# Kernel tuning notes

Measured on AMD Instinct MI355X. Metric: run time of the kernel, lower is better.

Reference implementation:

```python
import jax, jax.numpy as jnp
import numpy as np

N = 8192
C_IN = 512
C_INTER = 128  # in_channels // unit_nums = 512 // 4


def setup_inputs() -> dict:
    key = jax.random.key(0)
    ks = jax.random.split(key, 6)
    x = jax.random.normal(ks[0], (N, C_IN), dtype=jnp.float32)
    # Linear weights init: normal(0, 0.01); biases zero. Stored as [in, out].
    Wg = 0.01 * jax.random.normal(ks[1], (C_IN, C_INTER), dtype=jnp.float32)
    Wt = 0.01 * jax.random.normal(ks[2], (C_IN, C_INTER), dtype=jnp.float32)
    Wp = 0.01 * jax.random.normal(ks[3], (C_IN, C_INTER), dtype=jnp.float32)
    bg = jnp.zeros((C_INTER,), dtype=jnp.float32)
    bt = jnp.zeros((C_INTER,), dtype=jnp.float32)
    bp = jnp.zeros((C_INTER,), dtype=jnp.float32)
    # 1x1 conv weight (1, 2*C_INTER, 1, 1) flattened: first half hits theta, second half phi
    wcat = 0.01 * jax.random.normal(ks[4], (2 * C_INTER,), dtype=jnp.float32)
    return {"x": x, "Wg": Wg, "bg": bg, "Wt": Wt, "bt": bt, "Wp": Wp, "bp": bp, "wcat": wcat}


def reference(x, Wg, bg, Wt, bt, Wp, bp, wcat):
    n = x.shape[0]
    g_x = x @ Wg + bg          # [N, C_inter]
    theta = x @ Wt + bt        # [N, C_inter]
    phi = x @ Wp + bp          # [N, C_inter]
    c = theta.shape[1]
    # 1x1 conv over cat([theta_i, phi_j]) == w1.theta_i + w2.phi_j (outer sum), then ReLU
    a = theta @ wcat[:c]       # [N]
    b = phi @ wcat[c:]         # [N]
    f = jax.nn.relu(a[:, None] + b[None, :])  # [N, N]
    z = (f / n) @ g_x          # [N, C_inter]
    return z
```

## Files before the change

### kernel.cpp

```cpp
#include <hip/hip_runtime.h>

#define C_IN   512
#define C_INT  128
#define NBUCK  8192
#define NSEG   256
#define BPS    (NBUCK / NSEG)

typedef short short8 __attribute__((ext_vector_type(8)));
typedef float floatx4 __attribute__((ext_vector_type(4)));


__device__ __forceinline__ int bucket_of(float v, float bmin, float inv_w) {
    float fk = (v - bmin) * inv_w;
    fk = fminf(fmaxf(fk, 0.f), (float)(NBUCK - 1));
    return (int)fk;
}

__device__ __forceinline__ short bf16rnd(float v) {
    unsigned u = __float_as_uint(v);
    return (short)((u + 0x7fffu + ((u >> 16) & 1u)) >> 16);
}


__global__ __launch_bounds__(256) void prep_kernel(
        const float* __restrict__ Wt, const float* __restrict__ Wp,
        const float* __restrict__ Wg, const float* __restrict__ wcat,
        const float* __restrict__ bt, const float* __restrict__ bp,
        float* __restrict__ ut, float* __restrict__ up, float* __restrict__ scal,
        unsigned short* __restrict__ WgT) {
    int t = threadIdx.x, bk = blockIdx.x;
    if (bk < 16) {
        const float* W  = (bk < 8) ? Wt : Wp;
        const float* wv = wcat + ((bk < 8) ? 0 : C_INT);
        float* dst      = (bk < 8) ? ut : up;
        int k = (bk & 7) * 64 + (t >> 2);
        int q = t & 3;
        const float4* row = (const float4*)(W + (size_t)k * C_INT);
        const float4* cv4 = (const float4*)wv;
        float s = 0.f;
        #pragma unroll
        for (int i = 0; i < 8; ++i) {
            float4 a = row[q * 8 + i];
            float4 c = cv4[q * 8 + i];
            s += a.x * c.x + a.y * c.y + a.z * c.z + a.w * c.w;
        }
        s += __shfl_xor(s, 1);
        s += __shfl_xor(s, 2);
        if (q == 0) dst[k] = s;
    } else if (bk == 16) {
        float s1p = (t < C_INT) ? bt[t] * wcat[t] : 0.f;
        float s2p = (t < C_INT) ? bp[t] * wcat[C_INT + t] : 0.f;
        for (int off = 32; off; off >>= 1) {
            s1p += __shfl_down(s1p, off);
            s2p += __shfl_down(s2p, off);
        }
        __shared__ float red[8];
        int w = t >> 6, lane = t & 63;
        if (lane == 0) { red[w] = s1p; red[4 + w] = s2p; }
        __syncthreads();
        if (t == 0) {
            scal[0] = red[0] + red[1] + red[2] + red[3];
            scal[1] = red[4] + red[5] + red[6] + red[7];
        }
    } else {
        __shared__ float tile[64][132];
        int kb = (bk - 17) * 64;
        #pragma unroll
        for (int it = 0; it < 8; ++it) {
            int idx = it * 256 + t;
            int r = idx >> 5, c4 = idx & 31;
            *(float4*)&tile[r][c4 * 4] =
                ((const float4*)(Wg + (size_t)(kb + r) * C_INT))[c4];
        }
        __syncthreads();
        int n = t & 127, kc = (t >> 7) * 32;
        unsigned pk[16];
        #pragma unroll
        for (int i = 0; i < 16; ++i) {
            unsigned lo = (unsigned short)bf16rnd(tile[kc + 2 * i][n]);
            unsigned hi = (unsigned short)bf16rnd(tile[kc + 2 * i + 1][n]);
            pk[i] = lo | (hi << 16);
        }
        uint4* dst = (uint4*)(WgT + (size_t)n * C_IN + kb + kc);
        #pragma unroll
        for (int i2 = 0; i2 < 4; ++i2) dst[i2] = *(uint4*)&pk[i2 * 4];
    }
}


#define RSTR 66

__global__ __launch_bounds__(256) void gemm_mfma(
        const float* __restrict__ x, const unsigned short* __restrict__ WgT,
        const float* __restrict__ bg,
        const float* __restrict__ ut, const float* __restrict__ up,
        const float* __restrict__ scal,
        _Float16* __restrict__ g, float* __restrict__ a, float* __restrict__ b) {
    __shared__ float red[3][20][RSTR];
    int tid = threadIdx.x;
    int lane = tid & 63, wv = tid >> 6;
    int bx = blockIdx.x;
    int i0 = (bx >> 1) * 16;
    int cg = bx & 1;
    int m = lane & 15, q = lane >> 4;
    floatx4 accg[4] = {};
    floatx4 accab = {};
    const float* xrow = x + (size_t)(i0 + m) * C_IN + q * 8;
    const float* absrc = (m == 0) ? ut : up;
    #pragma unroll
    for (int ks = 0; ks < 4; ++ks) {
        int k0 = (wv * 4 + ks) * 32;
        float4 f0 = *(const float4*)(xrow + k0);
        float4 f1 = *(const float4*)(xrow + k0 + 4);
        short8 af;
        af[0] = bf16rnd(f0.x); af[1] = bf16rnd(f0.y);
        af[2] = bf16rnd(f0.z); af[3] = bf16rnd(f0.w);
        af[4] = bf16rnd(f1.x); af[5] = bf16rnd(f1.y);
        af[6] = bf16rnd(f1.z); af[7] = bf16rnd(f1.w);
        if (cg == 0) {
            short8 abf = {};
            if (m < 2) {
                float4 u0 = *(const float4*)(absrc + k0 + q * 8);
                float4 u1 = *(const float4*)(absrc + k0 + q * 8 + 4);
                abf[0] = bf16rnd(u0.x); abf[1] = bf16rnd(u0.y);
                abf[2] = bf16rnd(u0.z); abf[3] = bf16rnd(u0.w);
                abf[4] = bf16rnd(u1.x); abf[5] = bf16rnd(u1.y);
                abf[6] = bf16rnd(u1.z); abf[7] = bf16rnd(u1.w);
            }
            accab = __builtin_amdgcn_mfma_f32_16x16x32_bf16(af, abf, accab, 0, 0, 0);
        }
        #pragma unroll
        for (int f = 0; f < 4; ++f) {
            short8 bfr = *(const short8*)(WgT + (size_t)(cg * 64 + f * 16 + m) * C_IN + k0 + q * 8);
            accg[f] = __builtin_amdgcn_mfma_f32_16x16x32_bf16(af, bfr, accg[f], 0, 0, 0);
        }
    }
    if (wv) {
        #pragma unroll
        for (int f = 0; f < 4; ++f)
            #pragma unroll
            for (int r = 0; r < 4; ++r)
                red[wv - 1][f * 4 + r][lane] = accg[f][r];
        #pragma unroll
        for (int r = 0; r < 4; ++r)
            red[wv - 1][16 + r][lane] = accab[r];
    }
    __syncthreads();
    if (wv == 0) {
        #pragma unroll
        for (int w = 0; w < 3; ++w) {
            #pragma unroll
            for (int f = 0; f < 4; ++f)
                #pragma unroll
                for (int r = 0; r < 4; ++r)
                    accg[f][r] += red[w][f * 4 + r][lane];
            #pragma unroll
            for (int r = 0; r < 4; ++r)
                accab[r] += red[w][16 + r][lane];
        }
        #pragma unroll
        for (int f = 0; f < 4; ++f) {
            int col = cg * 64 + f * 16 + m;
            float bgv = bg[col];
            #pragma unroll
            for (int r = 0; r < 4; ++r) {
                int row = i0 + q * 4 + r;
                g[(size_t)row * C_INT + col] = (_Float16)(accg[f][r] + bgv);
            }
        }
        if (cg == 0 && m < 2) {
            float off = m ? scal[1] : scal[0];
            float* dst = m ? b : a;
            #pragma unroll
            for (int r = 0; r < 4; ++r) dst[i0 + q * 4 + r] = accab[r] + off;
        }
    }
}


__global__ __launch_bounds__(1024) void postA_kernel(
        const _Float16* __restrict__ g, const float* __restrict__ b,
        float* __restrict__ scal,
        unsigned* __restrict__ offs_g, unsigned short* __restrict__ perm_g,
        float* __restrict__ bsort_g,
        float* __restrict__ seg1, float* __restrict__ seg2) {
    __shared__ unsigned oh[NBUCK / 2];
    __shared__ unsigned cur[NBUCK / 2];
    __shared__ unsigned short ls[8192];
    __shared__ unsigned wtu[16];
    __shared__ float smn[16], smx[16];
    __shared__ float part1[8][128], part2[8][128];
    int t = threadIdx.x, s = blockIdx.x;
    int lane = t & 63, wv = t >> 6;
    #pragma unroll
    for (int r = 0; r < 4; ++r) { oh[t + r * 1024] = 0u; cur[t + r * 1024] = 0u; }
    float bv[8];
    float mn = 1e30f, mx = -1e30f;
    #pragma unroll
    for (int r = 0; r < 8; ++r) {
        bv[r] = b[t + r * 1024];
        mn = fminf(mn, bv[r]); mx = fmaxf(mx, bv[r]);
    }
    for (int off = 32; off; off >>= 1) {
        mn = fminf(mn, __shfl_down(mn, off));
        mx = fmaxf(mx, __shfl_down(mx, off));
    }
    if (lane == 0) { smn[wv] = mn; smx[wv] = mx; }
    __syncthreads();
    if (t == 0) {
        float gmn = smn[0], gmx = smx[0];
        #pragma unroll
        for (int i = 1; i < 16; ++i) {
            gmn = fminf(gmn, smn[i]); gmx = fmaxf(gmx, smx[i]);
        }
        float range = gmx - gmn;
        float iw = (range > 1e-30f) ? (float)NBUCK / range : 0.f;
        smn[0] = gmn; smx[0] = iw;
        if (s == 0) { scal[4] = gmn; scal[5] = iw; }
    }
    __syncthreads();
    float bmin = smn[0], inv_w = smx[0];
    int kb[8];
    #pragma unroll
    for (int r = 0; r < 8; ++r) {
        kb[r] = bucket_of(bv[r], bmin, inv_w);
        atomicAdd(&oh[kb[r] >> 1], (kb[r] & 1) ? 0x10000u : 1u);
    }
    __syncthreads();
    unsigned h[8], p0 = 0;
    #pragma unroll
    for (int w = 0; w < 4; ++w) {
        unsigned word = oh[t * 4 + w];
        p0 += word & 0xffffu;  h[w * 2]     = p0;
        p0 += word >> 16;      h[w * 2 + 1] = p0;
    }
    unsigned v = p0;
    #pragma unroll
    for (int d = 1; d < 64; d <<= 1) {
        unsigned u = __shfl_up(v, d);
        if (lane >= d) v += u;
    }
    if (lane == 63) wtu[wv] = v;
    __syncthreads();
    if (t < 16) {
        unsigned w = wtu[t];
        #pragma unroll
        for (int d = 1; d < 16; d <<= 1) {
            unsigned u = __shfl_up(w, d);
            if (t >= d) w += u;
        }
        wtu[t] = w;
    }
    __syncthreads();
    unsigned base = (v - p0) + (wv ? wtu[wv - 1] : 0u);
    #pragma unroll
    for (int w = 0; w < 4; ++w) {
        unsigned lo = base + h[w * 2], hi = base + h[w * 2 + 1];
        oh[t * 4 + w] = lo | (hi << 16);
        if (s == 0) {
            offs_g[t * 8 + w * 2 + 1] = lo;
            offs_g[t * 8 + w * 2 + 2] = hi;
        }
    }
    if (s == 0 && t == 0) offs_g[0] = 0u;
    __syncthreads();
    #pragma unroll
    for (int r = 0; r < 8; ++r) {
        int j = t + r * 1024;
        int k = kb[r];
        unsigned st = 0u;
        if (k > 0) {
            unsigned word = oh[(k - 1) >> 1];
            st = ((k - 1) & 1) ? (word >> 16) : (word & 0xffffu);
        }
        unsigned old = atomicAdd(&cur[k >> 1], (k & 1) ? 0x10000u : 1u);
        unsigned pos = (k & 1) ? (old >> 16) : (old & 0xffffu);
        ls[st + pos] = (unsigned short)j;
    }
    __syncthreads();
    auto incl = [&](int kk) -> unsigned {
        unsigned word = oh[kk >> 1];
        return (kk & 1) ? (word >> 16) : (word & 0xffffu);
    };
    unsigned E0 = (s == 0) ? 0u : incl(s * BPS - 1);
    unsigned E1 = incl((s + 1) * BPS - 1);
    for (unsigned e = E0 + t; e < E1; e += 1024) {
        int j = ls[e];
        perm_g[e] = (unsigned short)j;
        bsort_g[e] = b[j];
    }
    int c = t & 127, p = t >> 7;
    float a1 = 0.f, a2 = 0.f;
    for (unsigned e = E0 + p; e < E1; e += 8) {
        int j = ls[e];
        float gv = (float)g[(size_t)j * C_INT + c];
        a1 += gv; a2 += b[j] * gv;
    }
    part1[p][c] = a1; part2[p][c] = a2;
    __syncthreads();
    if (p == 0) {
        float t1 = 0.f, t2 = 0.f;
        #pragma unroll
        for (int pp = 0; pp < 8; ++pp) { t1 += part1[pp][c]; t2 += part2[pp][c]; }
        seg1[s * C_INT + c] = t1;
        seg2[s * C_INT + c] = t2;
    }
}


__global__ __launch_bounds__(128) void postB_kernel(
        const _Float16* __restrict__ g, const unsigned* __restrict__ offs,
        const unsigned short* __restrict__ perm, const float* __restrict__ bsort,
        const float* __restrict__ seg1, const float* __restrict__ seg2,
        float* __restrict__ Pr1, float* __restrict__ Pr2) {
    __shared__ int pj[128];
    __shared__ float pb[128];
    int s = blockIdx.x, c = threadIdx.x;
    unsigned E0 = offs[s * BPS], E1 = offs[(s + 1) * BPS];
    float r1 = 0.f, r2 = 0.f;
    for (int s2 = s + 1; s2 < NSEG; ++s2) {
        r1 += seg1[s2 * C_INT + c];
        r2 += seg2[s2 * C_INT + c];
    }
    unsigned e = E1;
    while (e > E0) {
        unsigned cb = (e >= E0 + 128u) ? e - 128u : E0;
        unsigned cnt = e - cb;
        if ((unsigned)c < cnt) { pj[c] = perm[cb + c]; pb[c] = bsort[cb + c]; }
        __syncthreads();
        for (int r = (int)cnt - 1; r >= 0; --r) {
            float gv = (float)g[(size_t)pj[r] * C_INT + c];
            r1 += gv; r2 += pb[r] * gv;
            size_t idx = (size_t)(cb + r) * C_INT + c;
            Pr1[idx] = r1; Pr2[idx] = r2;
        }
        __syncthreads();
        e = cb;
    }
    if (s == 0) {
        Pr1[(size_t)8192 * C_INT + c] = 0.f;
        Pr2[(size_t)8192 * C_INT + c] = 0.f;
    }
}


__global__ __launch_bounds__(128) void out_kernel(
        const float* __restrict__ a, const float* __restrict__ scal,
        const _Float16* __restrict__ g,
        const unsigned* __restrict__ offs, const unsigned short* __restrict__ perm,
        const float* __restrict__ bsort,
        const float* __restrict__ Pr1, const float* __restrict__ Pr2,
        float* __restrict__ out, float inv_n) {
    __shared__ int pj[128];
    __shared__ float pb[128];
    int i = blockIdx.x, c = threadIdx.x;
    float ai = a[i], thr = -ai;
    float bmin = scal[4], inv_w = scal[5];
    int ki = bucket_of(thr, bmin, inv_w);
    unsigned e0 = offs[ki], e1 = offs[ki + 1];
    size_t base = (size_t)e1 * C_INT + c;
    float acc = ai * Pr1[base] + Pr2[base];
    for (unsigned be = e0; be < e1; be += 128) {
        unsigned cnt = min(128u, e1 - be);
        if ((unsigned)c < cnt) { pj[c] = perm[be + c]; pb[c] = bsort[be + c]; }
        __syncthreads();
        for (unsigned r = 0; r < cnt; ++r) {
            float bj = pb[r];
            if (bj > thr)
                acc += (ai + bj) * (float)g[(size_t)pj[r] * C_INT + c];
        }
        __syncthreads();
    }
    out[(size_t)i * C_INT + c] = acc * inv_n;
}


extern "C" void kernel_launch(void* const* d_in, const int* in_sizes, int n_in,
                              void* d_out, int out_size, void* d_ws, size_t ws_size,
                              hipStream_t stream) {
    const float* x    = (const float*)d_in[0];
    const float* Wg   = (const float*)d_in[1];
    const float* bg   = (const float*)d_in[2];
    const float* Wt   = (const float*)d_in[3];
    const float* bt   = (const float*)d_in[4];
    const float* Wp   = (const float*)d_in[5];
    const float* bp   = (const float*)d_in[6];
    const float* wcat = (const float*)d_in[7];
    float* out = (float*)d_out;
    int n = in_sizes[0] / C_IN;

    char* w = (char*)d_ws;
    size_t off = 0;
    auto alloc = [&](size_t bytes) -> void* {
        void* p = w + off;
        off += (bytes + 255) & ~(size_t)255;
        return p;
    };
    float*          ut    = (float*)alloc(C_IN * 4);
    float*          up    = (float*)alloc(C_IN * 4);
    float*          scal  = (float*)alloc(32);
    float*          a     = (float*)alloc((size_t)n * 4);
    float*          b     = (float*)alloc((size_t)n * 4);
    unsigned*       offs  = (unsigned*)alloc((size_t)(NBUCK + 1) * 4);
    unsigned short* perm  = (unsigned short*)alloc((size_t)n * 2);
    float*          bsort = (float*)alloc((size_t)n * 4);
    _Float16*       g     = (_Float16*)alloc((size_t)n * C_INT * 2);
    unsigned short* WgT   = (unsigned short*)alloc((size_t)C_INT * C_IN * 2);
    float*          seg1  = (float*)alloc((size_t)NSEG * C_INT * 4);
    float*          seg2  = (float*)alloc((size_t)NSEG * C_INT * 4);
    float*          Pr1   = (float*)alloc((size_t)(n + 1) * C_INT * 4);
    float*          Pr2   = (float*)alloc((size_t)(n + 1) * C_INT * 4);

    prep_kernel<<<25, 256, 0, stream>>>(Wt, Wp, Wg, wcat, bt, bp, ut, up, scal, WgT);
    gemm_mfma<<<n / 8, 256, 0, stream>>>(x, WgT, bg, ut, up, scal, g, a, b);
    postA_kernel<<<NSEG, 1024, 0, stream>>>(g, b, scal, offs, perm, bsort, seg1, seg2);
    postB_kernel<<<NSEG, 128, 0, stream>>>(g, offs, perm, bsort, seg1, seg2, Pr1, Pr2);
    out_kernel<<<n, 128, 0, stream>>>(a, scal, g, offs, perm, bsort, Pr1, Pr2,
                                      out, 1.0f / (float)n);
}
```

Before: 143.5 us.

## Fuse bucketing, suffix-prefix and output stages into one cooperative kernel

Merges postA, postB and out_kernel into a single cooperative kernel with 256 blocks of 1024 threads, separated by grid-wide syncs. This removes two kernel launches and the global round trip for scalars, and reuses the shared-memory sorted list. In the fused version the per-segment suffix scan runs on only 128 threads per block. The output stage now has 1024 threads handle 32 rows per block, down from 8192 blocks of 128 threads, which reduces parallelism and leaves the irregular bucket loops serialized per thread.

```diff
diff --git a/kernel.cpp b/kernel.cpp
--- a/kernel.cpp
+++ b/kernel.cpp
@@ -1,4 +1,7 @@
 #include <hip/hip_runtime.h>
+#include <hip/hip_cooperative_groups.h>
+
+namespace cg = cooperative_groups;
 
 #define C_IN   512
 #define C_INT  128
@@ -101,7 +104,7 @@
     int lane = tid & 63, wv = tid >> 6;
     int bx = blockIdx.x;
     int i0 = (bx >> 1) * 16;
-    int cg = bx & 1;
+    int cg0 = bx & 1;
     int m = lane & 15, q = lane >> 4;
     floatx4 accg[4] = {};
     floatx4 accab = {};
@@ -117,7 +120,7 @@
         af[2] = bf16rnd(f0.z); af[3] = bf16rnd(f0.w);
         af[4] = bf16rnd(f1.x); af[5] = bf16rnd(f1.y);
         af[6] = bf16rnd(f1.z); af[7] = bf16rnd(f1.w);
-        if (cg == 0) {
+        if (cg0 == 0) {
             short8 abf = {};
             if (m < 2) {
                 float4 u0 = *(const float4*)(absrc + k0 + q * 8);
@@ -131,7 +134,7 @@
         }
         #pragma unroll
         for (int f = 0; f < 4; ++f) {
-            short8 bfr = *(const short8*)(WgT + (size_t)(cg * 64 + f * 16 + m) * C_IN + k0 + q * 8);
+            short8 bfr = *(const short8*)(WgT + (size_t)(cg0 * 64 + f * 16 + m) * C_IN + k0 + q * 8);
             accg[f] = __builtin_amdgcn_mfma_f32_16x16x32_bf16(af, bfr, accg[f], 0, 0, 0);
         }
     }
@@ -160,7 +163,7 @@
         }
         #pragma unroll
         for (int f = 0; f < 4; ++f) {
-            int col = cg * 64 + f * 16 + m;
+            int col = cg0 * 64 + f * 16 + m;
             float bgv = bg[col];
             #pragma unroll
             for (int r = 0; r < 4; ++r) {
@@ -168,7 +171,7 @@
                 g[(size_t)row * C_INT + col] = (_Float16)(accg[f][r] + bgv);
             }
         }
-        if (cg == 0 && m < 2) {
+        if (cg0 == 0 && m < 2) {
             float off = m ? scal[1] : scal[0];
             float* dst = m ? b : a;
             #pragma unroll
@@ -178,12 +181,15 @@
 }
 
 
-__global__ __launch_bounds__(1024) void postA_kernel(
+__global__ __launch_bounds__(1024) void mega_kernel(
         const _Float16* __restrict__ g, const float* __restrict__ b,
-        float* __restrict__ scal,
+        const float* __restrict__ a,
         unsigned* __restrict__ offs_g, unsigned short* __restrict__ perm_g,
         float* __restrict__ bsort_g,
-        float* __restrict__ seg1, float* __restrict__ seg2) {
+        float* __restrict__ seg1, float* __restrict__ seg2,
+        float* __restrict__ Pr1, float* __restrict__ Pr2,
+        float* __restrict__ out, float inv_n) {
+    cg::grid_group grid = cg::this_grid();
     __shared__ unsigned oh[NBUCK / 2];
     __shared__ unsigned cur[NBUCK / 2];
     __shared__ unsigned short ls[8192];
@@ -192,6 +198,8 @@
     __shared__ float part1[8][128], part2[8][128];
     int t = threadIdx.x, s = blockIdx.x;
     int lane = t & 63, wv = t >> 6;
+    int c = t & 127, p = t >> 7;
+
     #pragma unroll
     for (int r = 0; r < 4; ++r) { oh[t + r * 1024] = 0u; cur[t + r * 1024] = 0u; }
     float bv[8];
@@ -216,7 +224,6 @@
         float range = gmx - gmn;
         float iw = (range > 1e-30f) ? (float)NBUCK / range : 0.f;
         smn[0] = gmn; smx[0] = iw;
-        if (s == 0) { scal[4] = gmn; scal[5] = iw; }
     }
     __syncthreads();
     float bmin = smn[0], inv_w = smx[0];
@@ -289,89 +296,69 @@
         perm_g[e] = (unsigned short)j;
         bsort_g[e] = b[j];
     }
-    int c = t & 127, p = t >> 7;
-    float a1 = 0.f, a2 = 0.f;
-    for (unsigned e = E0 + p; e < E1; e += 8) {
-        int j = ls[e];
-        float gv = (float)g[(size_t)j * C_INT + c];
-        a1 += gv; a2 += b[j] * gv;
-    }
-    part1[p][c] = a1; part2[p][c] = a2;
-    __syncthreads();
-    if (p == 0) {
-        float t1 = 0.f, t2 = 0.f;
-        #pragma unroll
-        for (int pp = 0; pp < 8; ++pp) { t1 += part1[pp][c]; t2 += part2[pp][c]; }
-        seg1[s * C_INT + c] = t1;
-        seg2[s * C_INT + c] = t2;
-    }
-}
-
-
-__global__ __launch_bounds__(128) void postB_kernel(
-        const _Float16* __restrict__ g, const unsigned* __restrict__ offs,
-        const unsigned short* __restrict__ perm, const float* __restrict__ bsort,
-        const float* __restrict__ seg1, const float* __restrict__ seg2,
-        float* __restrict__ Pr1, float* __restrict__ Pr2) {
-    __shared__ int pj[128];
-    __shared__ float pb[128];
-    int s = blockIdx.x, c = threadIdx.x;
-    unsigned E0 = offs[s * BPS], E1 = offs[(s + 1) * BPS];
-    float r1 = 0.f, r2 = 0.f;
-    for (int s2 = s + 1; s2 < NSEG; ++s2) {
-        r1 += seg1[s2 * C_INT + c];
-        r2 += seg2[s2 * C_INT + c];
-    }
-    unsigned e = E1;
-    while (e > E0) {
-        unsigned cb = (e >= E0 + 128u) ? e - 128u : E0;
-        unsigned cnt = e - cb;
-        if ((unsigned)c < cnt) { pj[c] = perm[cb + c]; pb[c] = bsort[cb + c]; }
+    {
+        float a1 = 0.f, a2 = 0.f;
+        for (unsigned e = E0 + p; e < E1; e += 8) {
+            int j = ls[e];
+            float gv = (float)g[(size_t)j * C_INT + c];
+            a1 += gv; a2 += b[j] * gv;
+        }
+        part1[p][c] = a1; part2[p][c] = a2;
         __syncthreads();
-        for (int r = (int)cnt - 1; r >= 0; --r) {
-            float gv = (float)g[(size_t)pj[r] * C_INT + c];
-            r1 += gv; r2 += pb[r] * gv;
-            size_t idx = (size_t)(cb + r) * C_INT + c;
-            Pr1[idx] = r1; Pr2[idx] = r2;
-        }
-        __syncthreads();
-        e = cb;
-    }
-    if (s == 0) {
-        Pr1[(size_t)8192 * C_INT + c] = 0.f;
-        Pr2[(size_t)8192 * C_INT + c] = 0.f;
-    }
-}
-
-
-__global__ __launch_bounds__(128) void out_kernel(
-        const float* __restrict__ a, const float* __restrict__ scal,
-        const _Float16* __restrict__ g,
-        const unsigned* __restrict__ offs, const unsigned short* __restrict__ perm,
-        const float* __restrict__ bsort,
-        const float* __restrict__ Pr1, const float* __restrict__ Pr2,
-        float* __restrict__ out, float inv_n) {
-    __shared__ int pj[128];
-    __shared__ float pb[128];
-    int i = blockIdx.x, c = threadIdx.x;
-    float ai = a[i], thr = -ai;
-    float bmin = scal[4], inv_w = scal[5];
-    int ki = bucket_of(thr, bmin, inv_w);
-    unsigned e0 = offs[ki], e1 = offs[ki + 1];
-    size_t base = (size_t)e1 * C_INT + c;
-    float acc = ai * Pr1[base] + Pr2[base];
-    for (unsigned be = e0; be < e1; be += 128) {
-        unsigned cnt = min(128u, e1 - be);
-        if ((unsigned)c < cnt) { pj[c] = perm[be + c]; pb[c] = bsort[be + c]; }
-        __syncthreads();
-        for (unsigned r = 0; r < cnt; ++r) {
-            float bj = pb[r];
-            if (bj > thr)
-                acc += (ai + bj) * (float)g[(size_t)pj[r] * C_INT + c];
-        }
-        __syncthreads();
-    }
-    out[(size_t)i * C_INT + c] = acc * inv_n;
+        if (p == 0) {
+            float t1 = 0.f, t2 = 0.f;
+            #pragma unroll
+            for (int pp = 0; pp < 8; ++pp) { t1 += part1[pp][c]; t2 += part2[pp][c]; }
+            seg1[s * C_INT + c] = t1;
+            seg2[s * C_INT + c] = t2;
+        }
+    }
+    grid.sync();
+
+    {
+        float r1 = 0.f, r2 = 0.f;
+        for (int s2 = s + 1 + p; s2 < NSEG; s2 += 8) {
+            r1 += seg1[s2 * C_INT + c];
+            r2 += seg2[s2 * C_INT + c];
+        }
+        part1[p][c] = r1; part2[p][c] = r2;
+    }
+    __syncthreads();
+    if (t < 128) {
+        float w1 = 0.f, w2 = 0.f;
+        #pragma unroll
+        for (int pp = 0; pp < 8; ++pp) { w1 += part1[pp][t]; w2 += part2[pp][t]; }
+        for (int e = (int)E1 - 1; e >= (int)E0; --e) {
+            int j = ls[e];
+            float gv = (float)g[(size_t)j * C_INT + t];
+            w1 += gv; w2 += b[j] * gv;
+            size_t idx = (size_t)e * C_INT + t;
+            Pr1[idx] = w1; Pr2[idx] = w2;
+        }
+        if (s == 0) {
+            Pr1[(size_t)8192 * C_INT + t] = 0.f;
+            Pr2[(size_t)8192 * C_INT + t] = 0.f;
+        }
+    }
+    grid.sync();
+
+    #pragma unroll
+    for (int batch = 0; batch < 4; ++batch) {
+        int i = s * 32 + batch * 8 + p;
+        float ai = a[i], thr = -ai;
+        int ki = bucket_of(thr, bmin, inv_w);
+        unsigned e0 = offs_g[ki], e1 = offs_g[ki + 1];
+        size_t pb = (size_t)e1 * C_INT + c;
+        float acc = ai * Pr1[pb] + Pr2[pb];
+        for (unsigned e = e0; e < e1; ++e) {
+            float bj = bsort_g[e];
+            if (bj > thr) {
+                int j = perm_g[e];
+                acc += (ai + bj) * (float)g[(size_t)j * C_INT + c];
+            }
+        }
+        out[(size_t)i * C_INT + c] = acc * inv_n;
+    }
 }
 
 
@@ -413,8 +400,10 @@
 
     prep_kernel<<<25, 256, 0, stream>>>(Wt, Wp, Wg, wcat, bt, bp, ut, up, scal, WgT);
     gemm_mfma<<<n / 8, 256, 0, stream>>>(x, WgT, bg, ut, up, scal, g, a, b);
-    postA_kernel<<<NSEG, 1024, 0, stream>>>(g, b, scal, offs, perm, bsort, seg1, seg2);
-    postB_kernel<<<NSEG, 128, 0, stream>>>(g, offs, perm, bsort, seg1, seg2, Pr1, Pr2);
-    out_kernel<<<n, 128, 0, stream>>>(a, scal, g, offs, perm, bsort, Pr1, Pr2,
-                                      out, 1.0f / (float)n);
-}
+    float inv_n = 1.0f / (float)n;
+    void* kargs[] = {(void*)&g, (void*)&b, (void*)&a, (void*)&offs, (void*)&perm,
+                     (void*)&bsort, (void*)&seg1, (void*)&seg2, (void*)&Pr1,
+                     (void*)&Pr2, (void*)&out, (void*)&inv_n};
+    hipLaunchCooperativeKernel((void*)mega_kernel, dim3(NSEG), dim3(1024),
+                               kargs, 0, stream);
+}
```

Result: slower. 215.0 us (+49.8%).
